# Performance work log

Hardware: AMD Instinct MI355X
Metric: run time of the kernel (lower is better)

Reference implementation:

```python
import jax, jax.numpy as jnp
import numpy as np

L_LAYERS, N_TRACES, N_THETA = 250, 600, 30


def setup_inputs() -> dict:
    key = jax.random.key(0)
    k1, k2, k3, k4, k5 = jax.random.split(key, 5)
    # physically plausible elastic parameters (keeps asin args inside (-1,1))
    vp = 2500.0 + 1500.0 * jax.random.uniform(k1, (L_LAYERS, N_TRACES), dtype=jnp.float32)
    vs = vp * (0.45 + 0.1 * jax.random.uniform(k2, (L_LAYERS, N_TRACES), dtype=jnp.float32))
    rho = 2.2 + 0.4 * jax.random.uniform(k3, (L_LAYERS, N_TRACES), dtype=jnp.float32)
    # incidence angles in radians, up to ~31.5 degrees
    theta = jnp.sort(0.05 + 0.5 * jax.random.uniform(k4, (N_THETA,), dtype=jnp.float32))
    wavemat = 0.1 * jax.random.normal(k5, (L_LAYERS, L_LAYERS), dtype=jnp.float32)
    return {"vp": vp, "vs": vs, "rho": rho, "theta": theta, "wavemat": wavemat}


def reference(vp, vs, rho, theta, wavemat):
    # vp/vs/rho: [L, T]; theta: [A]; wavemat: [L, L]
    L, T = vp.shape
    A = theta.shape[0]
    # interface properties: upper (1) / lower (2) layer, shape [L-1, T, 1]
    a1, a2 = vp[:-1, :, None], vp[1:, :, None]
    b1, b2 = vs[:-1, :, None], vs[1:, :, None]
    r1, r2 = rho[:-1, :, None], rho[1:, :, None]
    th = theta[None, None, :]                      # [1, 1, A]
    p = jnp.sin(th) / a1                           # ray parameter, [L-1, T, A]
    shp = p.shape
    theta2 = jnp.arcsin(jnp.clip(p * a2, -1.0, 1.0))
    phi1 = jnp.arcsin(jnp.clip(p * b1, -1.0, 1.0))
    phi2 = jnp.arcsin(jnp.clip(p * b2, -1.0, 1.0))
    sth = jnp.broadcast_to(jnp.sin(th), shp)
    cth = jnp.broadcast_to(jnp.cos(th), shp)
    sth2, cth2 = jnp.sin(theta2), jnp.cos(theta2)
    sp1, cp1 = jnp.sin(phi1), jnp.cos(phi1)
    sp2, cp2 = jnp.sin(phi2), jnp.cos(phi2)
    q1 = r1 * b1 * (1.0 - 2.0 * sp1 ** 2)          # shear impedance terms
    q2 = r2 * b2 * (1.0 - 2.0 * sp2 ** 2)
    row_m2 = jnp.stack([2.0 * r1 * b1 * sp1 * cth, q1, 2.0 * r2 * b2 * sp2 * cth2, q2], axis=-1)
    # M, N: [L-1, T, A, 4, 4]
    M = jnp.stack([
        jnp.stack([-sth, -cp1, sth2, cp2], axis=-1),
        jnp.stack([cth, -sp1, cth2, -sp2], axis=-1),
        row_m2,
        jnp.stack([-r1 * a1 * (1.0 - 2.0 * sp1 ** 2), r1 * b1 * jnp.sin(2.0 * phi1),
                   r2 * a2 * (1.0 - 2.0 * sp2 ** 2), -r2 * b2 * jnp.sin(2.0 * phi2)], axis=-1),
    ], axis=-2)
    N = jnp.stack([
        jnp.stack([sth, cp1, -sth2, -cp2], axis=-1),
        jnp.stack([cth, -sp1, cth2, -sp2], axis=-1),
        row_m2,
        jnp.stack([r1 * a1 * (1.0 - 2.0 * sp1 ** 2), -r1 * b1 * jnp.sin(2.0 * phi1),
                   -r2 * a2 * (1.0 - 2.0 * sp2 ** 2), r2 * b2 * jnp.sin(2.0 * phi2)], axis=-1),
    ], axis=-2)
    # PdPu = (inv(M) @ N)[0, 0] == solve(M, N[:, 0])[0]
    rpp = jnp.linalg.solve(M, N[..., :, 0:1])[..., 0, 0]   # [L-1, T, A]
    ref = jnp.zeros((T, L, A), dtype=vp.dtype)
    ref = ref.at[:, : L - 1, :].set(jnp.moveaxis(rpp, 1, 0))
    # convolve with wavelet matrix per trace: [L, L] @ [T, L, A]
    cal_data = jnp.einsum('lk,tka->tla', wavemat, ref)
    return cal_data
```

## Files before the change

kernel.cpp:

```cpp
#include <hip/hip_runtime.h>

constexpr int L  = 250;
constexpr int T  = 600;
constexpr int A  = 30;

typedef _Float16 h8  __attribute__((ext_vector_type(8)));
typedef _Float16 h4  __attribute__((ext_vector_type(4)));
typedef float    f4  __attribute__((ext_vector_type(4)));

constexpr int RT_LD = 264;
constexpr int WA_LD = 264;

__global__ __launch_bounds__(256)
void zoep_fused(const float* __restrict__ vp,
                const float* __restrict__ vs,
                const float* __restrict__ rho,
                const float* __restrict__ theta,
                const float* __restrict__ wm,
                float* __restrict__ out)
{
    __shared__ alignas(16) _Float16 refT[32 * RT_LD];
    __shared__ alignas(16) _Float16 wmA[256 * WA_LD];
    __shared__ float sth_s[32];
    __shared__ float cth_s[32];

    const int tid = threadIdx.x;
    const int t   = blockIdx.x;

    if (tid < 32) {
        const float th = (tid < A) ? theta[tid] : 0.0f;
        sth_s[tid] = sinf(th);
        cth_s[tid] = cosf(th);
    }
    __syncthreads();

    const int  k     = tid;
    const bool valid = (k < L - 1);
    const int  kc    = valid ? k : (L - 2);

    const float a1 = vp[kc * T + t];
    const float a2 = vp[(kc + 1) * T + t];
    const float b1 = vs[kc * T + t];
    const float b2 = vs[(kc + 1) * T + t];
    const float r1 = rho[kc * T + t];
    const float r2 = rho[(kc + 1) * T + t];

    const float ra1  = __builtin_amdgcn_rcpf(a1);
    const float rb1  = r1 * b1, rb2 = r2 * b2;
    const float ra1r = r1 * a1, ra2r = r2 * a2;

#pragma unroll 2
    for (int a = 0; a < A; ++a) {
        const float sth = sth_s[a];
        const float cth = cth_s[a];

        const float p   = sth * ra1;
        const float s2  = p * a2;
        const float c2  = sqrtf(1.0f - s2 * s2);
        const float sp1 = p * b1;
        const float cp1 = sqrtf(1.0f - sp1 * sp1);
        const float sp2 = p * b2;
        const float cp2 = sqrtf(1.0f - sp2 * sp2);

        const float k1 = 1.0f - 2.0f * sp1 * sp1;
        const float k2 = 1.0f - 2.0f * sp2 * sp2;
        const float q1 = rb1 * k1;
        const float q2 = rb2 * k2;
        const float P1 = ra1r * k1;
        const float P2 = ra2r * k2;
        const float u1 = 2.0f * rb1 * sp1;
        const float u2 = 2.0f * rb2 * sp2;
        const float S1 = u1 * cp1;
        const float S2 = u2 * cp2;
        const float g1 = u1 * cth;
        const float g2 = u2 * c2;

        const float m00 = -sth, m01 = -cp1, m02 = s2,  m03 = cp2;
        const float m10 =  cth, m11 = -sp1, m12 = c2,  m13 = -sp2;
        const float m20 =  g1,  m21 =  q1,  m22 = g2,  m23 = q2;
        const float m30 = -P1,  m31 =  S1,  m32 = P2,  m33 = -S2;

        const float s3v = m01 * m12 - m11 * m02;
        const float s4v = m01 * m13 - m11 * m03;
        const float s5v = m02 * m13 - m12 * m03;
        const float c3v = m21 * m32 - m31 * m22;
        const float c4v = m21 * m33 - m31 * m23;
        const float c5v = m22 * m33 - m32 * m23;
        const float s0v = m00 * m11 - m10 * m01;
        const float s1v = m00 * m12 - m10 * m02;
        const float s2v = m00 * m13 - m10 * m03;
        const float c0v = m20 * m31 - m30 * m21;
        const float c1v = m20 * m32 - m30 * m22;
        const float c2v = m20 * m33 - m30 * m23;

        const float detM = s0v*c5v - s1v*c4v + s2v*c3v
                         + s3v*c2v - s4v*c1v + s5v*c0v;
        const float A0 = m11*c5v - m12*c4v + m13*c3v;
        const float A3 = m21*s5v - m22*s4v + m23*s3v;

        const float num = m00 * A0 - m30 * A3;
        const float res = 1.0f - 2.0f * num * __builtin_amdgcn_rcpf(detM);

        refT[a * RT_LD + k] = (_Float16)(valid ? res : 0.0f);
    }
    refT[30 * RT_LD + k] = (_Float16)0.0f;
    refT[31 * RT_LD + k] = (_Float16)0.0f;

    {
        const int cg = tid & 7;
        const int r0 = tid >> 3;
#pragma unroll
        for (int cs = 0; cs < 8; ++cs) {
#pragma unroll
            for (int p = 0; p < 8; ++p) {
                const int r  = p * 32 + r0;
                const int rc = (r < L) ? r : (L - 1);
                const int c0 = cs * 32 + cg * 4;
                const int c0c = (c0     <= L - 2) ? c0     : (L - 2);
                const int c1c = (c0 + 2 <= L - 2) ? c0 + 2 : (L - 2);
                const float2 f0 = *(const float2*)(wm + rc * L + c0c);
                const float2 f1 = *(const float2*)(wm + rc * L + c1c);
                h4 v;
                v[0] = (_Float16)((c0     < L) ? f0.x : 0.0f);
                v[1] = (_Float16)((c0 + 1 < L) ? f0.y : 0.0f);
                v[2] = (_Float16)((c0 + 2 < L) ? f1.x : 0.0f);
                v[3] = (_Float16)((c0 + 3 < L) ? f1.y : 0.0f);
                *(h4*)&wmA[r * WA_LD + c0] = v;
            }
        }
    }
    __syncthreads();

    const int w    = tid >> 6;
    const int lane = tid & 63;
    const int quad = lane >> 4;
    const int n16  = lane & 15;

    f4 acc[4][2];
#pragma unroll
    for (int mi = 0; mi < 4; ++mi)
#pragma unroll
        for (int nt = 0; nt < 2; ++nt) acc[mi][nt] = (f4){0.f, 0.f, 0.f, 0.f};

#pragma unroll
    for (int ks = 0; ks < 8; ++ks) {
        const int kofs = ks * 32 + quad * 8;
        const h8 b0 = *(const h8*)&refT[ n16       * RT_LD + kofs];
        const h8 b1 = *(const h8*)&refT[(16 + n16) * RT_LD + kofs];
#pragma unroll
        for (int mi = 0; mi < 4; ++mi) {
            const int m = (w * 4 + mi) * 16 + n16;
            const h8 af = *(const h8*)&wmA[m * WA_LD + kofs];
            acc[mi][0] = __builtin_amdgcn_mfma_f32_16x16x32_f16(af, b0, acc[mi][0], 0, 0, 0);
            acc[mi][1] = __builtin_amdgcn_mfma_f32_16x16x32_f16(af, b1, acc[mi][1], 0, 0, 0);
        }
    }

    float* outt = out + (size_t)t * (L * A);
#pragma unroll
    for (int mi = 0; mi < 4; ++mi) {
        const int mbase = (w * 4 + mi) * 16 + quad * 4;
#pragma unroll
        for (int nt = 0; nt < 2; ++nt) {
            const int a = nt * 16 + n16;
            if (a < A) {
#pragma unroll
                for (int r = 0; r < 4; ++r) {
                    const int l = mbase + r;
                    if (l < L) outt[l * A + a] = acc[mi][nt][r];
                }
            }
        }
    }
}

extern "C" void kernel_launch(void* const* d_in, const int* in_sizes, int n_in,
                              void* d_out, int out_size, void* d_ws, size_t ws_size,
                              hipStream_t stream) {
    (void)in_sizes; (void)n_in; (void)out_size; (void)d_ws; (void)ws_size;
    const float* vp    = (const float*)d_in[0];
    const float* vs    = (const float*)d_in[1];
    const float* rho   = (const float*)d_in[2];
    const float* theta = (const float*)d_in[3];
    const float* wm    = (const float*)d_in[4];
    float* out = (float*)d_out;

    zoep_fused<<<dim3(T), dim3(256), 0, stream>>>(vp, vs, rho, theta, wm, out);
}
```

Before: 113.3 us.

## Split output rows across two blocks per trace and alias shared buffers

Each trace is now handled by two blocks, each computing half of the wavelet-matrix rows. The reflectivity B fragments are preloaded into registers so the shared buffer can be reused for the half-size wavelet tile, shrinking LDS from about 150KB to about 68KB so two blocks can reside per CU. The cost is that the Zoeppritz solve is duplicated in both blocks and the B fragments add register pressure.

Result: no change. 112.8 us (-0.4%).

```diff
diff --git a/kernel.cpp b/kernel.cpp
--- a/kernel.cpp
+++ b/kernel.cpp
@@ -11,7 +11,7 @@
 constexpr int RT_LD = 264;
 constexpr int WA_LD = 264;
 
-__global__ __launch_bounds__(256)
+__global__ __launch_bounds__(256, 2)
 void zoep_fused(const float* __restrict__ vp,
                 const float* __restrict__ vs,
                 const float* __restrict__ rho,
@@ -19,13 +19,18 @@
                 const float* __restrict__ wm,
                 float* __restrict__ out)
 {
-    __shared__ alignas(16) _Float16 refT[32 * RT_LD];
-    __shared__ alignas(16) _Float16 wmA[256 * WA_LD];
+    __shared__ alignas(16) _Float16 smem[128 * WA_LD];
     __shared__ float sth_s[32];
     __shared__ float cth_s[32];
 
-    const int tid = threadIdx.x;
-    const int t   = blockIdx.x;
+    _Float16* const refT = smem;
+    _Float16* const wmA  = smem;
+
+    const int tid   = threadIdx.x;
+    const int bid   = blockIdx.x;
+    const int t     = bid >> 1;
+    const int mhalf = bid & 1;
+    const int mbase = mhalf * 128;
 
     if (tid < 32) {
         const float th = (tid < A) ? theta[tid] : 0.0f;
@@ -105,6 +110,21 @@
     }
     refT[30 * RT_LD + k] = (_Float16)0.0f;
     refT[31 * RT_LD + k] = (_Float16)0.0f;
+    __syncthreads();
+
+    const int w    = tid >> 6;
+    const int lane = tid & 63;
+    const int quad = lane >> 4;
+    const int n16  = lane & 15;
+
+    h8 bf[8][2];
+#pragma unroll
+    for (int ks = 0; ks < 8; ++ks) {
+        const int kofs = ks * 32 + quad * 8;
+        bf[ks][0] = *(const h8*)&refT[ n16       * RT_LD + kofs];
+        bf[ks][1] = *(const h8*)&refT[(16 + n16) * RT_LD + kofs];
+    }
+    __syncthreads();
 
     {
         const int cg = tid & 7;
@@ -112,14 +132,15 @@
 #pragma unroll
         for (int cs = 0; cs < 8; ++cs) {
 #pragma unroll
-            for (int p = 0; p < 8; ++p) {
+            for (int p = 0; p < 4; ++p) {
                 const int r  = p * 32 + r0;
-                const int rc = (r < L) ? r : (L - 1);
+                const int g  = mbase + r;
+                const int gc = (g < L) ? g : (L - 1);
                 const int c0 = cs * 32 + cg * 4;
                 const int c0c = (c0     <= L - 2) ? c0     : (L - 2);
                 const int c1c = (c0 + 2 <= L - 2) ? c0 + 2 : (L - 2);
-                const float2 f0 = *(const float2*)(wm + rc * L + c0c);
-                const float2 f1 = *(const float2*)(wm + rc * L + c1c);
+                const float2 f0 = *(const float2*)(wm + gc * L + c0c);
+                const float2 f1 = *(const float2*)(wm + gc * L + c1c);
                 h4 v;
                 v[0] = (_Float16)((c0     < L) ? f0.x : 0.0f);
                 v[1] = (_Float16)((c0 + 1 < L) ? f0.y : 0.0f);
@@ -131,42 +152,35 @@
     }
     __syncthreads();
 
-    const int w    = tid >> 6;
-    const int lane = tid & 63;
-    const int quad = lane >> 4;
-    const int n16  = lane & 15;
-
-    f4 acc[4][2];
-#pragma unroll
-    for (int mi = 0; mi < 4; ++mi)
+    f4 acc[2][2];
+#pragma unroll
+    for (int mi = 0; mi < 2; ++mi)
 #pragma unroll
         for (int nt = 0; nt < 2; ++nt) acc[mi][nt] = (f4){0.f, 0.f, 0.f, 0.f};
 
 #pragma unroll
     for (int ks = 0; ks < 8; ++ks) {
         const int kofs = ks * 32 + quad * 8;
-        const h8 b0 = *(const h8*)&refT[ n16       * RT_LD + kofs];
-        const h8 b1 = *(const h8*)&refT[(16 + n16) * RT_LD + kofs];
-#pragma unroll
-        for (int mi = 0; mi < 4; ++mi) {
-            const int m = (w * 4 + mi) * 16 + n16;
-            const h8 af = *(const h8*)&wmA[m * WA_LD + kofs];
-            acc[mi][0] = __builtin_amdgcn_mfma_f32_16x16x32_f16(af, b0, acc[mi][0], 0, 0, 0);
-            acc[mi][1] = __builtin_amdgcn_mfma_f32_16x16x32_f16(af, b1, acc[mi][1], 0, 0, 0);
+#pragma unroll
+        for (int mi = 0; mi < 2; ++mi) {
+            const int mloc = (w * 2 + mi) * 16 + n16;
+            const h8 af = *(const h8*)&wmA[mloc * WA_LD + kofs];
+            acc[mi][0] = __builtin_amdgcn_mfma_f32_16x16x32_f16(af, bf[ks][0], acc[mi][0], 0, 0, 0);
+            acc[mi][1] = __builtin_amdgcn_mfma_f32_16x16x32_f16(af, bf[ks][1], acc[mi][1], 0, 0, 0);
         }
     }
 
     float* outt = out + (size_t)t * (L * A);
 #pragma unroll
-    for (int mi = 0; mi < 4; ++mi) {
-        const int mbase = (w * 4 + mi) * 16 + quad * 4;
+    for (int mi = 0; mi < 2; ++mi) {
+        const int lbase = mbase + (w * 2 + mi) * 16 + quad * 4;
 #pragma unroll
         for (int nt = 0; nt < 2; ++nt) {
             const int a = nt * 16 + n16;
             if (a < A) {
 #pragma unroll
                 for (int r = 0; r < 4; ++r) {
-                    const int l = mbase + r;
+                    const int l = lbase + r;
                     if (l < L) outt[l * A + a] = acc[mi][nt][r];
                 }
             }
@@ -185,5 +199,5 @@
     const float* wm    = (const float*)d_in[4];
     float* out = (float*)d_out;
 
-    zoep_fused<<<dim3(T), dim3(256), 0, stream>>>(vp, vs, rho, theta, wm, out);
+    zoep_fused<<<dim3(2 * T), dim3(256), 0, stream>>>(vp, vs, rho, theta, wm, out);
 }
```
